# Kernel tuning notes

Hardware: AMD Instinct MI355X
Metric: run time of the kernel (lower is better)

The kernel has to match this reference:

```python
import jax, jax.numpy as jnp
import numpy as np

# Architecture constants (match init_kwargs)
L, M, K, P, G = 3, 4096, 2, 4, 4
NUM_IN, NUM_OUT, B = 8192, 1000, 2048
F = 6          # number of combinact activation functions
EPS_BN = 1e-5  # BatchNorm1d eps
EPS = 1e-12    # numeric safety for sqrt


def setup_inputs() -> dict:
    key = jax.random.key(0)
    ks = jax.random.split(key, 8)
    x = jax.random.normal(ks[0], (B, NUM_IN), jnp.float32)
    # shuffle maps: perm 0 is identity (the un-permuted copy), perms 1..P-1 random
    rng = np.random.default_rng(0)
    perms = np.stack([
        np.stack([np.arange(M)] + [rng.permutation(M) for _ in range(P - 1)])
        for _ in range(L)
    ]).astype(np.int32)  # (L, P, M)
    cin_g = NUM_IN // G  # per-group input width (curr stays 8192 every layer)
    W = jax.random.normal(ks[1], (L, G, M // G, cin_g), jnp.float32) / np.sqrt(cin_g)
    b = jax.random.normal(ks[2], (L, G, M // G), jnp.float32) * 0.01
    gamma = jnp.ones((L, M), jnp.float32)
    beta = jnp.zeros((L, M), jnp.float32)
    # original inits alpha_primes to zeros; small random gives non-degenerate mixing
    alpha = jax.random.normal(ks[3], (L, P, F), jnp.float32) * 0.1
    d_last = (M // K) * P
    W_out = jax.random.normal(ks[4], (NUM_OUT, d_last), jnp.float32) / np.sqrt(d_last)
    b_out = jnp.zeros((NUM_OUT,), jnp.float32)
    return {"x": x, "perms": jnp.asarray(perms), "W": W, "b": b,
            "gamma": gamma, "beta": beta, "alpha": alpha,
            "W_out": W_out, "b_out": b_out}


def _combinact(z, alpha_l):
    # z: (B, clusters, K, P) -> (B, clusters, P); per-perm softmax mixing
    sig = jax.nn.sigmoid(z)
    pr = jnp.prod(z, axis=2)
    acts = jnp.stack([
        jnp.max(z, axis=2),                          # max
        jnp.sign(pr) * jnp.sqrt(jnp.abs(pr) + EPS),  # signed geomean (k=2)
        z[:, :, 0, :] * jnp.prod(sig, axis=2),       # swish-k
        jnp.sqrt(jnp.sum(z * z, axis=2) + EPS),      # l2
        jnp.max(jnp.abs(z), axis=2),                 # linf
        jax.nn.logsumexp(z, axis=2),                 # lse
    ], axis=0)  # (F, B, clusters, P)
    w = jax.nn.softmax(alpha_l, axis=-1)  # (P, F)
    return jnp.einsum('fbcp,pf->bcp', acts, w)


def _forward(x, perms, W, b, gamma, beta, alpha, W_out, b_out):
    h = x
    for l in range(L):
        C = h.shape[1]
        # grouped small linears: (B, C/G, G) x (G, M/G, C/G) -> (B, M/G, G) -> (B, M)
        hr = h.reshape(B, C // G, G)
        y = jnp.einsum('bcg,gmc->bmg', hr, W[l]) + b[l].T[None]
        y = y.reshape(B, M)
        # BatchNorm1d (training mode, biased batch var)
        mu = jnp.mean(y, axis=0)
        var = jnp.mean((y - mu) ** 2, axis=0)
        y = (y - mu) * jax.lax.rsqrt(var + EPS_BN) * gamma[l] + beta[l]
        # p permuted copies, reshape into clusters of k
        zc = y[:, perms[l]]                                   # (B, P, M) gather
        z = jnp.transpose(zc, (0, 2, 1)).reshape(B, M // K, K, P)
        a = _combinact(z, alpha[l])                           # (B, M/K, P)
        h = jnp.transpose(a, (0, 2, 1)).reshape(B, (M // K) * P)
    return h @ W_out.T + b_out


def reference(x, perms, W, b, gamma, beta, alpha, W_out, b_out):
    return _forward(x, perms, W, b, gamma, beta, alpha, W_out, b_out)
```

## Files before the change

kernel.cpp:

```cpp
#include <hip/hip_runtime.h>
#include <math.h>

#define Lnum 3
#define Mdim 4096
#define Pdim 4
#define Gdim 4
#define NIN 8192
#define NOUT 1000
#define Bdim 2048
#define Fdim 6
#define CIN 2048
#define MG 1024
#define CH 2048
#define DNEXT 8192
#define NRCHUNK (Bdim / 128)

typedef short bf16x8 __attribute__((ext_vector_type(8)));
typedef float f32x4 __attribute__((ext_vector_type(4)));

__device__ __forceinline__ short f2bf(float f) {
    union { float f; unsigned u; } v; v.f = f;
    unsigned u = v.u;
    unsigned r = (u + 0x7fffu + ((u >> 16) & 1u)) >> 16;
    return (short)r;
}
__device__ __forceinline__ float bf2f(short h) {
    union { unsigned u; float f; } x;
    x.u = ((unsigned)(unsigned short)h) << 16;
    return x.f;
}

__global__ __launch_bounds__(256) void convert_f32_bf16(
    const float* __restrict__ src, short* __restrict__ dst, int n8)
{
    int i = blockIdx.x * 256 + threadIdx.x;
    if (i >= n8) return;
    const float4* s = (const float4*)src + (size_t)i * 2;
    float4 v0 = s[0], v1 = s[1];
    bf16x8 o;
    o[0] = f2bf(v0.x); o[1] = f2bf(v0.y); o[2] = f2bf(v0.z); o[3] = f2bf(v0.w);
    o[4] = f2bf(v1.x); o[5] = f2bf(v1.y); o[6] = f2bf(v1.z); o[7] = f2bf(v1.w);
    *((bf16x8*)dst + i) = o;
}

__global__ __launch_bounds__(256) void convert_wo(
    const float* __restrict__ src, short* __restrict__ dst)
{
    int i = blockIdx.x * 256 + threadIdx.x;
    int row = i >> 10;
    bf16x8 o;
    if (row < NOUT) {
        const float4* s = (const float4*)(src + (size_t)row * DNEXT + (i & 1023) * 8);
        float4 v0 = s[0], v1 = s[1];
        o[0] = f2bf(v0.x); o[1] = f2bf(v0.y); o[2] = f2bf(v0.z); o[3] = f2bf(v0.w);
        o[4] = f2bf(v1.x); o[5] = f2bf(v1.y); o[6] = f2bf(v1.z); o[7] = f2bf(v1.w);
    } else {
        for (int j = 0; j < 8; ++j) o[j] = 0;
    }
    *((bf16x8*)dst + i) = o;
}

__global__ __launch_bounds__(256) void x_to_grouped(
    const float* __restrict__ x, short* __restrict__ hg)
{
    const int c = blockIdx.x * 256 + threadIdx.x;
    const int b = blockIdx.y;
    float4 v = *(const float4*)(x + (size_t)b * NIN + 4 * c);
    const size_t plane = (size_t)Bdim * CIN;
    hg[0 * plane + (size_t)b * CIN + c] = f2bf(v.x);
    hg[1 * plane + (size_t)b * CIN + c] = f2bf(v.y);
    hg[2 * plane + (size_t)b * CIN + c] = f2bf(v.z);
    hg[3 * plane + (size_t)b * CIN + c] = f2bf(v.w);
}

__global__ __launch_bounds__(256) void remap_perms(
    const int* __restrict__ perm, int* __restrict__ perm_g, int n)
{
    int i = blockIdx.x * 256 + threadIdx.x;
    if (i >= n) return;
    int j = perm[i];
    perm_g[i] = ((j & 3) << 10) | (j >> 2);
}

template<int BN_T, int NWARP, bool STATS, typename CT>
__global__ __launch_bounds__(NWARP * 64) void gemm_mfma(
    const short* __restrict__ A0, size_t aZ, int lda,
    const short* __restrict__ B0, size_t bZ, int ldb,
    const float* __restrict__ bias0, size_t biasZ,
    CT* __restrict__ C0, size_t cZ,
    int K, int ldc, int nbound,
    float* __restrict__ psum, float* __restrict__ psumsq, int sgz)
{
    constexpr int NT   = NWARP * 64;
    constexpr int WCN  = NWARP / 2;
    constexpr int WCOL = BN_T / WCN;
    constexpr int FN   = WCOL / 16;

    const int nx = gridDim.x, ny = gridDim.y;
    const int nwg = nx * ny * gridDim.z;
    const int lin = blockIdx.x + nx * (blockIdx.y + ny * blockIdx.z);
    int swz = (lin & 7) * (nwg >> 3) + (lin >> 3);
    const int bx = swz % nx; swz /= nx;
    const int by = swz % ny;
    const int g  = swz / ny;

    const short* A  = A0 + aZ * g;
    const short* Bm = B0 + bZ * g;
    CT* C = C0 + cZ * g;

    const int n0 = bx * BN_T;
    const int b0 = by * 128;

    __shared__ short As[2][128 * 64];
    __shared__ short Bs[2][BN_T * 64];

    const int tid  = threadIdx.x;
    const int w    = tid >> 6;
    const int lane = tid & 63;
    const int wr = w / WCN, wc = w % WCN;

    f32x4 acc[4][FN];
#pragma unroll
    for (int m = 0; m < 4; ++m)
#pragma unroll
        for (int n = 0; n < FN; ++n) acc[m][n] = (f32x4)0.f;

    auto stage = [&](int buf, int k0) {
#pragma unroll
        for (int idx = tid; idx < 128 * 8; idx += NT) {
            const int r = idx >> 3, slot = idx & 7;
            const int gs = slot ^ (r & 7);
            const short* ga = A + (size_t)(b0 + r) * lda + k0 + gs * 8;
            __builtin_amdgcn_global_load_lds(
                (const __attribute__((address_space(1))) void*)ga,
                (__attribute__((address_space(3))) void*)(&As[buf][idx * 8]), 16, 0, 0);
        }
#pragma unroll
        for (int idx = tid; idx < BN_T * 8; idx += NT) {
            const int r = idx >> 3, slot = idx & 7;
            const int gs = slot ^ (r & 7);
            const short* gb = Bm + (size_t)(n0 + r) * ldb + k0 + gs * 8;
            __builtin_amdgcn_global_load_lds(
                (const __attribute__((address_space(1))) void*)gb,
                (__attribute__((address_space(3))) void*)(&Bs[buf][idx * 8]), 16, 0, 0);
        }
    };

    const int fr15 = lane & 15;
    const int fq   = lane >> 4;

    auto compute = [&](int buf) {
#pragma unroll
        for (int kk = 0; kk < 2; ++kk) {
            bf16x8 af[4], bff[FN];
            const int kob = kk * 64 + fq * 16;
#pragma unroll
            for (int m = 0; m < 4; ++m) {
                const int r  = wr * 64 + m * 16 + fr15;
                const int sw = kob ^ ((r & 7) << 4);
                af[m] = *(const bf16x8*)(&As[buf][r * 64 + (sw >> 1)]);
            }
#pragma unroll
            for (int n = 0; n < FN; ++n) {
                const int r  = wc * WCOL + n * 16 + fr15;
                const int sw = kob ^ ((r & 7) << 4);
                bff[n] = *(const bf16x8*)(&Bs[buf][r * 64 + (sw >> 1)]);
            }
#pragma unroll
            for (int m = 0; m < 4; ++m)
#pragma unroll
                for (int n = 0; n < FN; ++n)
                    acc[m][n] = __builtin_amdgcn_mfma_f32_16x16x32_bf16(af[m], bff[n], acc[m][n], 0, 0, 0);
        }
    };

    stage(0, 0);

    const int nt = K >> 6;
    int p = 0;
    for (int t = 0; t < nt - 1; ++t) {
        stage(p ^ 1, (t + 1) << 6);
        asm volatile("s_waitcnt vmcnt(4)" ::: "memory");
        __builtin_amdgcn_s_barrier();
        asm volatile("" ::: "memory");
        compute(p);
        asm volatile("" ::: "memory");
        __builtin_amdgcn_s_barrier();
        p ^= 1;
    }
    asm volatile("s_waitcnt vmcnt(0)" ::: "memory");
    __builtin_amdgcn_s_barrier();
    asm volatile("" ::: "memory");
    compute(p);

    float s[FN], ss[FN];
#pragma unroll
    for (int n = 0; n < FN; ++n) { s[n] = 0.f; ss[n] = 0.f; }

#pragma unroll
    for (int m = 0; m < 4; ++m) {
#pragma unroll
        for (int n = 0; n < FN; ++n) {
#pragma unroll
            for (int j = 0; j < 4; ++j) {
                const int row = b0 + wr * 64 + m * 16 + fq * 4 + j;
                const int col = n0 + wc * WCOL + n * 16 + fr15;
                if (col < nbound) {
                    float v = acc[m][n][j];
                    if (bias0) v += bias0[biasZ * g + col];
                    C[(size_t)row * ldc + col] = (CT)(sizeof(CT) == 2 ? (CT)f2bf(v) : (CT)v);
                    if (STATS) { s[n] += v; ss[n] += v * v; }
                }
            }
        }
    }

    if (STATS) {
        __syncthreads();
        float* sum_lds = (float*)&As[0][0];
        float* ssq_lds = sum_lds + BN_T * 8;
        const int slot = wr * 4 + fq;
#pragma unroll
        for (int n = 0; n < FN; ++n) {
            const int cl = wc * WCOL + n * 16 + fr15;
            sum_lds[cl * 8 + slot] = s[n];
            ssq_lds[cl * 8 + slot] = ss[n];
        }
        __syncthreads();
        for (int cl = tid; cl < BN_T; cl += NT) {
            float a = 0.f, b = 0.f;
#pragma unroll
            for (int q = 0; q < 8; ++q) {
                a += sum_lds[cl * 8 + q];
                b += ssq_lds[cl * 8 + q];
            }
            const size_t o = (size_t)by * Mdim + g * sgz + n0 + cl;
            psum[o]   = a;
            psumsq[o] = b;
        }
    }
}

__global__ __launch_bounds__(256) void reduce_out(
    const float* __restrict__ part, const float* __restrict__ bo,
    float* __restrict__ out)
{
    const int n = blockIdx.x * 256 + threadIdx.x;
    const int b = blockIdx.y;
    if (n >= NOUT) return;
    const size_t S = (size_t)Bdim * 1024;
    const size_t i = (size_t)b * 1024 + n;
    out[(size_t)b * NOUT + n] =
        part[i] + part[S + i] + part[2 * S + i] + part[3 * S + i] + bo[n];
}

__global__ __launch_bounds__(256) void bn_finalize(
    const float* __restrict__ psum, const float* __restrict__ psumsq,
    const float* __restrict__ gamma, const float* __restrict__ beta,
    float* __restrict__ scale, float* __restrict__ shift)
{
    const int jg = blockIdx.x * 256 + threadIdx.x;
    if (jg >= Mdim) return;
    const int j = ((jg & 1023) << 2) | (jg >> 10);
    float s = 0.f, ss = 0.f;
    for (int r = 0; r < NRCHUNK; ++r) {
        s  += psum[r * Mdim + jg];
        ss += psumsq[r * Mdim + jg];
    }
    const float mu  = s * (1.f / Bdim);
    const float var = ss * (1.f / Bdim) - mu * mu;
    const float sc  = gamma[j] * rsqrtf(var + 1e-5f);
    scale[jg] = sc;
    shift[jg] = beta[j] - mu * sc;
}

__global__ void alpha_softmax(const float* __restrict__ alpha, float* __restrict__ wsm)
{
    const int idx = threadIdx.x;
    if (idx >= Lnum * Pdim) return;
    const float* a = alpha + idx * Fdim;
    float mx = a[0];
#pragma unroll
    for (int f = 1; f < Fdim; ++f) mx = fmaxf(mx, a[f]);
    float e[Fdim]; float s = 0.f;
#pragma unroll
    for (int f = 0; f < Fdim; ++f) { e[f] = __expf(a[f] - mx); s += e[f]; }
    const float inv = 1.f / s;
#pragma unroll
    for (int f = 0; f < Fdim; ++f) wsm[idx * Fdim + f] = e[f] * inv;
}

template<int MODE>
__global__ __launch_bounds__(256) void combinact_kernel(
    const short* __restrict__ Y, const float* __restrict__ scale,
    const float* __restrict__ shift, const int* __restrict__ perm,
    const float* __restrict__ wsm, short* __restrict__ out)
{
    __shared__ float yn[Mdim];
    const int b   = blockIdx.x;
    const int tid = threadIdx.x;

#pragma unroll
    for (int k = 0; k < 2; ++k) {
        const int i8 = k * 256 + tid;
        bf16x8 v = *((const bf16x8*)(Y + (size_t)b * Mdim) + i8);
        float4 sc0 = *(const float4*)(scale + i8 * 8);
        float4 sc1 = *(const float4*)(scale + i8 * 8 + 4);
        float4 sh0 = *(const float4*)(shift + i8 * 8);
        float4 sh1 = *(const float4*)(shift + i8 * 8 + 4);
        float* o = yn + i8 * 8;
        o[0] = bf2f(v[0]) * sc0.x + sh0.x;
        o[1] = bf2f(v[1]) * sc0.y + sh0.y;
        o[2] = bf2f(v[2]) * sc0.z + sh0.z;
        o[3] = bf2f(v[3]) * sc0.w + sh0.w;
        o[4] = bf2f(v[4]) * sc1.x + sh1.x;
        o[5] = bf2f(v[5]) * sc1.y + sh1.y;
        o[6] = bf2f(v[6]) * sc1.z + sh1.z;
        o[7] = bf2f(v[7]) * sc1.w + sh1.w;
    }
    __syncthreads();

    float wv[Pdim][Fdim];
#pragma unroll
    for (int p = 0; p < Pdim; ++p)
#pragma unroll
        for (int f = 0; f < Fdim; ++f) wv[p][f] = wsm[p * Fdim + f];

    const float L2E = 1.44269504f;
    const float LN2 = 0.69314718f;

#pragma unroll
    for (int k = 0; k < 8; ++k) {
        const int idx = k * 256 + tid;
        int c, g = 0, q = 0;
        if (MODE == 0) { g = idx >> 9; q = idx & 511; c = q * 4 + g; }
        else           { c = idx; }

#pragma unroll
        for (int p = 0; p < Pdim; ++p) {
            const int2 jj = *(const int2*)(perm + p * Mdim + 2 * c);
            const float z0 = yn[jj.x];
            const float z1 = yn[jj.y];

            const float mx = fmaxf(z0, z1);
            const float pr = z0 * z1;
            const float a1 = copysignf(__builtin_amdgcn_sqrtf(fabsf(pr) + 1e-12f), pr);

            const float e0 = __builtin_amdgcn_exp2f(-L2E * z0);
            const float e1 = __builtin_amdgcn_exp2f(-L2E * z1);
            const float a2 = z0 * __builtin_amdgcn_rcpf((1.f + e0) * (1.f + e1));

            const float a3 = __builtin_amdgcn_sqrtf(z0 * z0 + z1 * z1 + 1e-12f);
            const float a4 = fmaxf(fabsf(z0), fabsf(z1));

            const float ed = __builtin_amdgcn_exp2f(-L2E * fabsf(z0 - z1));
            const float a5 = mx + LN2 * __builtin_amdgcn_logf(1.f + ed);

            const float v = wv[p][0] * mx + wv[p][1] * a1 + wv[p][2] * a2 +
                            wv[p][3] * a3 + wv[p][4] * a4 + wv[p][5] * a5;

            if (MODE == 0)
                out[(size_t)g * ((size_t)Bdim * CIN) + (size_t)b * CIN + p * 512 + q] = f2bf(v);
            else
                out[(size_t)b * DNEXT + p * CH + c] = f2bf(v);
        }
    }
}

extern "C" void kernel_launch(void* const* d_in, const int* in_sizes, int n_in,
                              void* d_out, int out_size, void* d_ws, size_t ws_size,
                              hipStream_t stream)
{
    const float* x     = (const float*)d_in[0];
    const int*   perms = (const int*)  d_in[1];
    const float* W     = (const float*)d_in[2];
    const float* bvec  = (const float*)d_in[3];
    const float* gamma = (const float*)d_in[4];
    const float* beta  = (const float*)d_in[5];
    const float* alpha = (const float*)d_in[6];
    const float* Wo    = (const float*)d_in[7];
    const float* bo    = (const float*)d_in[8];
    float* out = (float*)d_out;

    char* ws = (char*)d_ws;
    short* y      = (short*)ws;
    short* hg     = y + (size_t)Bdim * Mdim;
    short* Wlb3   = hg + (size_t)Gdim * Bdim * CIN;
    short* Wob    = Wlb3 + (size_t)Lnum * Gdim * MG * CIN;
    float* psum   = (float*)(Wob + (size_t)1024 * DNEXT);
    float* psumsq = psum + (size_t)NRCHUNK * Mdim;
    float* scale  = psumsq + (size_t)NRCHUNK * Mdim;
    float* shift  = scale + Mdim;
    float* wsm    = shift + Mdim;
    int*   perm_g = (int*)(wsm + Lnum * Pdim * Fdim);

    short* hflat = hg;
    float* part  = (float*)Wlb3;

    alpha_softmax<<<1, 64, 0, stream>>>(alpha, wsm);
    remap_perms<<<(Lnum * Pdim * Mdim) / 256, 256, 0, stream>>>(
        perms, perm_g, Lnum * Pdim * Mdim);
    convert_f32_bf16<<<(Lnum * Gdim * MG * CIN / 8) / 256, 256, 0, stream>>>(
        W, Wlb3, Lnum * Gdim * MG * CIN / 8);
    convert_wo<<<(1024 * 1024) / 256, 256, 0, stream>>>(Wo, Wob);
    x_to_grouped<<<dim3(CIN / 256, Bdim), 256, 0, stream>>>(x, hg);

    const size_t planeA = (size_t)Bdim * CIN;
    const size_t planeB = (size_t)MG * CIN;

    for (int l = 0; l < Lnum; ++l) {
        dim3 gg(MG / 128, Bdim / 128, Gdim);
        gemm_mfma<128, 8, true, short><<<gg, 512, 0, stream>>>(
            hg, planeA, CIN, Wlb3 + (size_t)l * Gdim * MG * CIN, planeB, CIN,
            bvec + (size_t)l * Gdim * MG, (size_t)MG,
            y, (size_t)MG,
            CIN, Mdim, MG,
            psum, psumsq, MG);

        bn_finalize<<<Mdim / 256, 256, 0, stream>>>(
            psum, psumsq, gamma + (size_t)l * Mdim, beta + (size_t)l * Mdim, scale, shift);

        if (l < Lnum - 1)
            combinact_kernel<0><<<Bdim, 256, 0, stream>>>(
                y, scale, shift, perm_g + (size_t)l * Pdim * Mdim, wsm + l * Pdim * Fdim, hg);
        else
            combinact_kernel<1><<<Bdim, 256, 0, stream>>>(
                y, scale, shift, perm_g + (size_t)l * Pdim * Mdim, wsm + l * Pdim * Fdim, hflat);
    }

    dim3 go(1024 / 128, Bdim / 128, 4);
    gemm_mfma<128, 8, false, float><<<go, 512, 0, stream>>>(
        hflat, (size_t)2048, DNEXT, Wob, (size_t)2048, DNEXT,
        nullptr, 0,
        part, (size_t)Bdim * 1024,
        2048, 1024, 1024,
        nullptr, nullptr, 0);

    dim3 gr(4, Bdim);
    reduce_out<<<gr, 256, 0, stream>>>(part, bo, out);
}
```

Baseline: 312.7 us.

## Process four batch rows per combinact block with swizzled float4 LDS layout

The combinact kernel now handles four batch rows per workgroup. Normalized values are stored in LDS as float4 vectors (one lane per row), so each permutation index lookup and LDS gather serves four rows, which amortizes the perm index loads and the scale/shift loads. The permutation remap XOR-swizzles indices to match a swizzled LDS write pattern and reduce bank conflicts. In exchange, LDS use rises to 64KB per block, which lowers occupancy, and the grid shrinks to a quarter of the blocks.

Measured after the change: 316.2 us. About the same (+1.1%).

```diff
diff --git a/kernel.cpp b/kernel.cpp
--- a/kernel.cpp
+++ b/kernel.cpp
@@ -78,8 +78,9 @@
 {
     int i = blockIdx.x * 256 + threadIdx.x;
     if (i >= n) return;
-    int j = perm[i];
-    perm_g[i] = ((j & 3) << 10) | (j >> 2);
+    int j  = perm[i];
+    int jg = ((j & 3) << 10) | (j >> 2);
+    perm_g[i] = jg ^ ((jg >> 3) & 3);
 }
 
 template<int BN_T, int NWARP, bool STATS, typename CT>
@@ -296,27 +297,30 @@
     const float* __restrict__ shift, const int* __restrict__ perm,
     const float* __restrict__ wsm, short* __restrict__ out)
 {
-    __shared__ float yn[Mdim];
-    const int b   = blockIdx.x;
+    __shared__ f32x4 yn4[Mdim];
+    const int b0  = blockIdx.x * 4;
     const int tid = threadIdx.x;
 
 #pragma unroll
     for (int k = 0; k < 2; ++k) {
-        const int i8 = k * 256 + tid;
-        bf16x8 v = *((const bf16x8*)(Y + (size_t)b * Mdim) + i8);
-        float4 sc0 = *(const float4*)(scale + i8 * 8);
-        float4 sc1 = *(const float4*)(scale + i8 * 8 + 4);
-        float4 sh0 = *(const float4*)(shift + i8 * 8);
-        float4 sh1 = *(const float4*)(shift + i8 * 8 + 4);
-        float* o = yn + i8 * 8;
-        o[0] = bf2f(v[0]) * sc0.x + sh0.x;
-        o[1] = bf2f(v[1]) * sc0.y + sh0.y;
-        o[2] = bf2f(v[2]) * sc0.z + sh0.z;
-        o[3] = bf2f(v[3]) * sc0.w + sh0.w;
-        o[4] = bf2f(v[4]) * sc1.x + sh1.x;
-        o[5] = bf2f(v[5]) * sc1.y + sh1.y;
-        o[6] = bf2f(v[6]) * sc1.z + sh1.z;
-        o[7] = bf2f(v[7]) * sc1.w + sh1.w;
+        const int i8   = k * 256 + tid;
+        const int base = i8 * 8;
+        const bf16x8 v0 = *((const bf16x8*)(Y + (size_t)(b0 + 0) * Mdim) + i8);
+        const bf16x8 v1 = *((const bf16x8*)(Y + (size_t)(b0 + 1) * Mdim) + i8);
+        const bf16x8 v2 = *((const bf16x8*)(Y + (size_t)(b0 + 2) * Mdim) + i8);
+        const bf16x8 v3 = *((const bf16x8*)(Y + (size_t)(b0 + 3) * Mdim) + i8);
+        const int xr = i8 & 3;
+#pragma unroll
+        for (int jj = 0; jj < 8; ++jj) {
+            const float sc = scale[base + jj];
+            const float sh = shift[base + jj];
+            f32x4 t;
+            t[0] = bf2f(v0[jj]) * sc + sh;
+            t[1] = bf2f(v1[jj]) * sc + sh;
+            t[2] = bf2f(v2[jj]) * sc + sh;
+            t[3] = bf2f(v3[jj]) * sc + sh;
+            yn4[base + (jj ^ xr)] = t;
+        }
     }
     __syncthreads();
 
@@ -328,6 +332,7 @@
 
     const float L2E = 1.44269504f;
     const float LN2 = 0.69314718f;
+    const size_t plane = (size_t)Bdim * CIN;
 
 #pragma unroll
     for (int k = 0; k < 8; ++k) {
@@ -339,30 +344,36 @@
 #pragma unroll
         for (int p = 0; p < Pdim; ++p) {
             const int2 jj = *(const int2*)(perm + p * Mdim + 2 * c);
-            const float z0 = yn[jj.x];
-            const float z1 = yn[jj.y];
-
-            const float mx = fmaxf(z0, z1);
-            const float pr = z0 * z1;
-            const float a1 = copysignf(__builtin_amdgcn_sqrtf(fabsf(pr) + 1e-12f), pr);
-
-            const float e0 = __builtin_amdgcn_exp2f(-L2E * z0);
-            const float e1 = __builtin_amdgcn_exp2f(-L2E * z1);
-            const float a2 = z0 * __builtin_amdgcn_rcpf((1.f + e0) * (1.f + e1));
-
-            const float a3 = __builtin_amdgcn_sqrtf(z0 * z0 + z1 * z1 + 1e-12f);
-            const float a4 = fmaxf(fabsf(z0), fabsf(z1));
-
-            const float ed = __builtin_amdgcn_exp2f(-L2E * fabsf(z0 - z1));
-            const float a5 = mx + LN2 * __builtin_amdgcn_logf(1.f + ed);
-
-            const float v = wv[p][0] * mx + wv[p][1] * a1 + wv[p][2] * a2 +
-                            wv[p][3] * a3 + wv[p][4] * a4 + wv[p][5] * a5;
-
-            if (MODE == 0)
-                out[(size_t)g * ((size_t)Bdim * CIN) + (size_t)b * CIN + p * 512 + q] = f2bf(v);
-            else
-                out[(size_t)b * DNEXT + p * CH + c] = f2bf(v);
+            const f32x4 z0v = yn4[jj.x];
+            const f32x4 z1v = yn4[jj.y];
+
+#pragma unroll
+            for (int r = 0; r < 4; ++r) {
+                const float z0 = z0v[r];
+                const float z1 = z1v[r];
+
+                const float mx = fmaxf(z0, z1);
+                const float pr = z0 * z1;
+                const float a1 = copysignf(__builtin_amdgcn_sqrtf(fabsf(pr) + 1e-12f), pr);
+
+                const float e0 = __builtin_amdgcn_exp2f(-L2E * z0);
+                const float e1 = __builtin_amdgcn_exp2f(-L2E * z1);
+                const float a2 = z0 * __builtin_amdgcn_rcpf((1.f + e0) * (1.f + e1));
+
+                const float a3 = __builtin_amdgcn_sqrtf(z0 * z0 + z1 * z1 + 1e-12f);
+                const float a4 = fmaxf(fabsf(z0), fabsf(z1));
+
+                const float ed = __builtin_amdgcn_exp2f(-L2E * fabsf(z0 - z1));
+                const float a5 = mx + LN2 * __builtin_amdgcn_logf(1.f + ed);
+
+                const float v = wv[p][0] * mx + wv[p][1] * a1 + wv[p][2] * a2 +
+                                wv[p][3] * a3 + wv[p][4] * a4 + wv[p][5] * a5;
+
+                if (MODE == 0)
+                    out[g * plane + (size_t)(b0 + r) * CIN + p * 512 + q] = f2bf(v);
+                else
+                    out[(size_t)(b0 + r) * DNEXT + p * CH + c] = f2bf(v);
+            }
         }
     }
 }
@@ -421,10 +432,10 @@
             psum, psumsq, gamma + (size_t)l * Mdim, beta + (size_t)l * Mdim, scale, shift);
 
         if (l < Lnum - 1)
-            combinact_kernel<0><<<Bdim, 256, 0, stream>>>(
+            combinact_kernel<0><<<Bdim / 4, 256, 0, stream>>>(
                 y, scale, shift, perm_g + (size_t)l * Pdim * Mdim, wsm + l * Pdim * Fdim, hg);
         else
-            combinact_kernel<1><<<Bdim, 256, 0, stream>>>(
+            combinact_kernel<1><<<Bdim / 4, 256, 0, stream>>>(
                 y, scale, shift, perm_g + (size_t)l * Pdim * Mdim, wsm + l * Pdim * Fdim, hflat);
     }
 
```
